# Optimization experiments

Hardware: AMD Instinct MI355X
Metric: run time of the kernel (lower is better)

Reference implementation:

```python
import jax, jax.numpy as jnp
import numpy as np

DT = 1.0
SPIKE_THRESHOLD = 30.0


def setup_inputs() -> dict:
    key = jax.random.key(0)
    kx, = jax.random.split(key, 1)
    x = jax.random.normal(kx, (16, 64, 1024, 32), dtype=jnp.float32)
    # scalar learnable parameters (Izhikevich model constants)
    a = jnp.float32(0.02)
    b = jnp.float32(0.2)
    c = jnp.float32(-65.0)
    d = jnp.float32(8.0)
    return {"x": x, "a": a, "b": b, "c": c, "d": d}


def reference(x, a, b, c, d):
    # x: [B, C, N, T]. Initial membrane potential v and recovery u are zeros.
    B, C, N, T = x.shape
    v0 = jnp.zeros((B, C, N), dtype=x.dtype)
    u0 = jnp.zeros((B, C, N), dtype=x.dtype)
    xs = jnp.moveaxis(x, -1, 0)  # [T, B, C, N] time-major for scan

    def step(carry, x_t):
        v, u = carry
        dv = 0.04 * v * v + 5.0 * v + 140.0 - u + x_t
        v = v + DT * dv
        du = a * (b * v - u)
        u = u + DT * du
        spike = (v >= SPIKE_THRESHOLD).astype(x_t.dtype)
        v = v * (1.0 - spike) + c * spike
        u = u + d * spike
        return (v, u), spike

    (_, _), spikes = jax.lax.scan(step, (v0, u0), xs)
    return jnp.moveaxis(spikes, 0, -1)  # [B, C, N, T]
```

## Files before the change

kernel.cpp:

```cpp
#include <hip/hip_runtime.h>


#define T_STEPS 32
#define TPB 64
#define ROW 36

__global__ __launch_bounds__(TPB) void izhikevich_kernel(
    const float* __restrict__ x,
    const float* __restrict__ pa,
    const float* __restrict__ pb,
    const float* __restrict__ pc,
    const float* __restrict__ pd,
    float* __restrict__ out)
{
#pragma clang fp contract(off)
    __shared__ float lds[TPB * ROW];

    const int t = threadIdx.x;
    const size_t base = (size_t)blockIdx.x * (TPB * T_STEPS);

    const float a = pa[0];
    const float b = pb[0];
    const float c = pc[0];
    const float d = pd[0];

    const float4* __restrict__ xin = reinterpret_cast<const float4*>(x + base);
    float4 ch[8];
#pragma unroll
    for (int k = 0; k < 8; ++k) ch[k] = xin[k * TPB + t];

#pragma unroll
    for (int k = 0; k < 8; ++k) {
        const int ng = k * 8 + (t >> 3);
        const int tg = (t & 7) * 4;
        *reinterpret_cast<float4*>(&lds[ng * ROW + tg]) = ch[k];
    }
    __syncthreads();

    float xs[T_STEPS];
#pragma unroll
    for (int j = 0; j < 8; ++j)
        *reinterpret_cast<float4*>(&xs[j * 4]) =
            *reinterpret_cast<const float4*>(&lds[t * ROW + j * 4]);

    float v = 0.0f;
    float u = 0.0f;
#pragma unroll
    for (int j = 0; j < 8; ++j) {
        float4 sp;
        float* sf = reinterpret_cast<float*>(&sp);
#pragma unroll
        for (int i = 0; i < 4; ++i) {
            const float xt = xs[j * 4 + i];
            const float t1 = (0.04f * v) * v;
            const float t2 = 5.0f * v;
            const float dv = (((t1 + t2) + 140.0f) - u) + xt;
            v = v + dv;
            const float du = a * ((b * v) - u);
            u = u + du;
            const float spike = (v >= 30.0f) ? 1.0f : 0.0f;
            const float oms = 1.0f - spike;
            v = (v * oms) + (c * spike);
            u = u + (d * spike);
            sf[i] = spike;
        }
        *reinterpret_cast<float4*>(&lds[t * ROW + j * 4]) = sp;
    }
    __syncthreads();

    float4* __restrict__ op = reinterpret_cast<float4*>(out + base);
#pragma unroll
    for (int k = 0; k < 8; ++k) {
        const int ng = k * 8 + (t >> 3);
        const int tg = (t & 7) * 4;
        const float4 o = *reinterpret_cast<const float4*>(&lds[ng * ROW + tg]);
        op[k * TPB + t] = o;
    }
}

extern "C" void kernel_launch(void* const* d_in, const int* in_sizes, int n_in,
                              void* d_out, int out_size, void* d_ws, size_t ws_size,
                              hipStream_t stream) {
    const float* x  = (const float*)d_in[0];
    const float* pa = (const float*)d_in[1];
    const float* pb = (const float*)d_in[2];
    const float* pc = (const float*)d_in[3];
    const float* pd = (const float*)d_in[4];
    float* out = (float*)d_out;

    const int n_neurons = in_sizes[0] / T_STEPS;
    const int grid = n_neurons / TPB;

    izhikevich_kernel<<<grid, TPB, 0, stream>>>(x, pa, pb, pc, pd, out);
}
```

Measured before the change: 236.9 us.

## Process four tiles per block with register prefetch of the next tile

Each block now handles four consecutive 64-neuron tiles, prefetching the next tile's input into registers while computing the current one, and cuts the grid by four. Because the block is a single wavefront, __syncthreads is replaced by explicit s_waitcnt lgkmcnt(0) waits. The aim is to overlap global loads with compute and amortize per-block launch and setup costs. In exchange there are fewer resident waves for latency hiding and higher register pressure from the extra 8 float4 buffer. There is also a risk of LDS write-after-read hazards across wave instructions, since only lgkmcnt is awaited.

```diff
diff --git a/kernel.cpp b/kernel.cpp
--- a/kernel.cpp
+++ b/kernel.cpp
@@ -4,6 +4,7 @@
 #define T_STEPS 32
 #define TPB 64
 #define ROW 36
+#define NT 4
 
 __global__ __launch_bounds__(TPB) void izhikevich_kernel(
     const float* __restrict__ x,
@@ -17,64 +18,88 @@
     __shared__ float lds[TPB * ROW];
 
     const int t = threadIdx.x;
-    const size_t base = (size_t)blockIdx.x * (TPB * T_STEPS);
+    const size_t tile_elems = (size_t)TPB * T_STEPS;
+    const size_t base0 = (size_t)blockIdx.x * (NT * tile_elems);
 
     const float a = pa[0];
     const float b = pb[0];
     const float c = pc[0];
     const float d = pd[0];
 
-    const float4* __restrict__ xin = reinterpret_cast<const float4*>(x + base);
     float4 ch[8];
+    {
+        const float4* __restrict__ xin = reinterpret_cast<const float4*>(x + base0);
 #pragma unroll
-    for (int k = 0; k < 8; ++k) ch[k] = xin[k * TPB + t];
+        for (int k = 0; k < 8; ++k) ch[k] = xin[k * TPB + t];
+    }
 
 #pragma unroll
-    for (int k = 0; k < 8; ++k) {
-        const int ng = k * 8 + (t >> 3);
-        const int tg = (t & 7) * 4;
-        *reinterpret_cast<float4*>(&lds[ng * ROW + tg]) = ch[k];
-    }
-    __syncthreads();
+    for (int it = 0; it < NT; ++it) {
+#pragma unroll
+        for (int k = 0; k < 8; ++k) {
+            const int ng = k * 8 + (t >> 3);
+            const int tg = (t & 7) * 4;
+            *reinterpret_cast<float4*>(&lds[ng * ROW + tg]) = ch[k];
+        }
 
-    float xs[T_STEPS];
+        float4 chn[8];
+        if (it + 1 < NT) {
+            const float4* __restrict__ xin =
+                reinterpret_cast<const float4*>(x + base0 + (size_t)(it + 1) * tile_elems);
 #pragma unroll
-    for (int j = 0; j < 8; ++j)
-        *reinterpret_cast<float4*>(&xs[j * 4]) =
-            *reinterpret_cast<const float4*>(&lds[t * ROW + j * 4]);
+            for (int k = 0; k < 8; ++k) chn[k] = xin[k * TPB + t];
+        }
 
-    float v = 0.0f;
-    float u = 0.0f;
+        asm volatile("s_waitcnt lgkmcnt(0)" ::: "memory");
+
+        float xs[T_STEPS];
 #pragma unroll
-    for (int j = 0; j < 8; ++j) {
-        float4 sp;
-        float* sf = reinterpret_cast<float*>(&sp);
+        for (int j = 0; j < 8; ++j)
+            *reinterpret_cast<float4*>(&xs[j * 4]) =
+                *reinterpret_cast<const float4*>(&lds[t * ROW + j * 4]);
+
+        float v = 0.0f;
+        float u = 0.0f;
 #pragma unroll
-        for (int i = 0; i < 4; ++i) {
-            const float xt = xs[j * 4 + i];
-            const float t1 = (0.04f * v) * v;
-            const float t2 = 5.0f * v;
-            const float dv = (((t1 + t2) + 140.0f) - u) + xt;
-            v = v + dv;
-            const float du = a * ((b * v) - u);
-            u = u + du;
-            const float spike = (v >= 30.0f) ? 1.0f : 0.0f;
-            const float oms = 1.0f - spike;
-            v = (v * oms) + (c * spike);
-            u = u + (d * spike);
-            sf[i] = spike;
+        for (int j = 0; j < 8; ++j) {
+            float4 sp;
+            float* sf = reinterpret_cast<float*>(&sp);
+#pragma unroll
+            for (int i = 0; i < 4; ++i) {
+                const float xt = xs[j * 4 + i];
+                const float t1 = (0.04f * v) * v;
+                const float t2 = 5.0f * v;
+                const float dv = (((t1 + t2) + 140.0f) - u) + xt;
+                v = v + dv;
+                const float du = a * ((b * v) - u);
+                u = u + du;
+                const float spike = (v >= 30.0f) ? 1.0f : 0.0f;
+                const float oms = 1.0f - spike;
+                v = (v * oms) + (c * spike);
+                u = u + (d * spike);
+                sf[i] = spike;
+            }
+            *reinterpret_cast<float4*>(&lds[t * ROW + j * 4]) = sp;
         }
-        *reinterpret_cast<float4*>(&lds[t * ROW + j * 4]) = sp;
-    }
-    __syncthreads();
 
-    float4* __restrict__ op = reinterpret_cast<float4*>(out + base);
+        asm volatile("s_waitcnt lgkmcnt(0)" ::: "memory");
+
+        {
+            float4* __restrict__ op =
+                reinterpret_cast<float4*>(out + base0 + (size_t)it * tile_elems);
 #pragma unroll
-    for (int k = 0; k < 8; ++k) {
-        const int ng = k * 8 + (t >> 3);
-        const int tg = (t & 7) * 4;
-        const float4 o = *reinterpret_cast<const float4*>(&lds[ng * ROW + tg]);
-        op[k * TPB + t] = o;
+            for (int k = 0; k < 8; ++k) {
+                const int ng = k * 8 + (t >> 3);
+                const int tg = (t & 7) * 4;
+                const float4 o = *reinterpret_cast<const float4*>(&lds[ng * ROW + tg]);
+                op[k * TPB + t] = o;
+            }
+        }
+
+        if (it + 1 < NT) {
+#pragma unroll
+            for (int k = 0; k < 8; ++k) ch[k] = chn[k];
+        }
     }
 }
 
@@ -89,7 +114,7 @@
     float* out = (float*)d_out;
 
     const int n_neurons = in_sizes[0] / T_STEPS;
-    const int grid = n_neurons / TPB;
+    const int grid = n_neurons / (TPB * NT);
 
     izhikevich_kernel<<<grid, TPB, 0, stream>>>(x, pa, pb, pc, pd, out);
 }
```

Result: slower. 242.2 us (+2.2%).

## Drop LDS transpose, load and store each neuron's row directly with nontemporal stores

Applied to the files above, without the earlier changes.

Removes the shared-memory staging transpose and both barriers. Each thread now reads its neuron's 32 contiguous floats as eight float4 loads and writes its spikes back the same way using nontemporal stores. Block size goes from 64 to 256. The cost is that each global access is strided by 128 bytes across lanes instead of fully coalesced, which relies on the cache to merge the per-thread row accesses.

```diff
diff --git a/kernel.cpp b/kernel.cpp
--- a/kernel.cpp
+++ b/kernel.cpp
@@ -2,8 +2,9 @@
 
 
 #define T_STEPS 32
-#define TPB 64
-#define ROW 36
+#define TPB 256
+
+typedef float vf4 __attribute__((ext_vector_type(4)));
 
 __global__ __launch_bounds__(TPB) void izhikevich_kernel(
     const float* __restrict__ x,
@@ -14,44 +15,28 @@
     float* __restrict__ out)
 {
 #pragma clang fp contract(off)
-    __shared__ float lds[TPB * ROW];
-
-    const int t = threadIdx.x;
-    const size_t base = (size_t)blockIdx.x * (TPB * T_STEPS);
+    const size_t neuron = (size_t)blockIdx.x * TPB + threadIdx.x;
+    const float* __restrict__ xp = x + neuron * T_STEPS;
+    float* __restrict__ op = out + neuron * T_STEPS;
 
     const float a = pa[0];
     const float b = pb[0];
     const float c = pc[0];
     const float d = pd[0];
 
-    const float4* __restrict__ xin = reinterpret_cast<const float4*>(x + base);
-    float4 ch[8];
+    vf4 xv[8];
 #pragma unroll
-    for (int k = 0; k < 8; ++k) ch[k] = xin[k * TPB + t];
-
-#pragma unroll
-    for (int k = 0; k < 8; ++k) {
-        const int ng = k * 8 + (t >> 3);
-        const int tg = (t & 7) * 4;
-        *reinterpret_cast<float4*>(&lds[ng * ROW + tg]) = ch[k];
-    }
-    __syncthreads();
-
-    float xs[T_STEPS];
-#pragma unroll
-    for (int j = 0; j < 8; ++j)
-        *reinterpret_cast<float4*>(&xs[j * 4]) =
-            *reinterpret_cast<const float4*>(&lds[t * ROW + j * 4]);
+    for (int k = 0; k < 8; ++k)
+        xv[k] = *reinterpret_cast<const vf4*>(xp + 4 * k);
 
     float v = 0.0f;
     float u = 0.0f;
+    vf4 sp[8];
 #pragma unroll
     for (int j = 0; j < 8; ++j) {
-        float4 sp;
-        float* sf = reinterpret_cast<float*>(&sp);
 #pragma unroll
         for (int i = 0; i < 4; ++i) {
-            const float xt = xs[j * 4 + i];
+            const float xt = xv[j][i];
             const float t1 = (0.04f * v) * v;
             const float t2 = 5.0f * v;
             const float dv = (((t1 + t2) + 140.0f) - u) + xt;
@@ -62,20 +47,13 @@
             const float oms = 1.0f - spike;
             v = (v * oms) + (c * spike);
             u = u + (d * spike);
-            sf[i] = spike;
+            sp[j][i] = spike;
         }
-        *reinterpret_cast<float4*>(&lds[t * ROW + j * 4]) = sp;
     }
-    __syncthreads();
 
-    float4* __restrict__ op = reinterpret_cast<float4*>(out + base);
 #pragma unroll
-    for (int k = 0; k < 8; ++k) {
-        const int ng = k * 8 + (t >> 3);
-        const int tg = (t & 7) * 4;
-        const float4 o = *reinterpret_cast<const float4*>(&lds[ng * ROW + tg]);
-        op[k * TPB + t] = o;
-    }
+    for (int k = 0; k < 8; ++k)
+        __builtin_nontemporal_store(sp[k], reinterpret_cast<vf4*>(op + 4 * k));
 }
 
 extern "C" void kernel_launch(void* const* d_in, const int* in_sizes, int n_in,
```

Result: slower. 551.1 us (+132.7%).
